# Performance work log

Hardware: AMD Instinct MI355X
Metric: run time of the kernel (lower is better)

Reference implementation:

```python
import jax, jax.numpy as jnp
import numpy as np

EPS = 1e-12


def _segment_softmax(logits, seg, n):
    # numerically stable softmax over edges grouped by destination node
    m = jax.ops.segment_max(logits, seg, num_segments=n)
    e = jnp.exp(logits - m[seg])
    s = jax.ops.segment_sum(e, seg, num_segments=n)
    return e / s[seg]


def _agnn(x, src, dst, beta, n):
    # cosine-similarity attention (PyG AGNNConv): alpha_ij = softmax_i(beta * <x_i/|x_i|, x_j/|x_j|>)
    norm = jnp.sqrt(jnp.sum(x * x, axis=-1, keepdims=True))
    xn = x / jnp.maximum(norm, EPS)
    logits = beta * jnp.sum(xn[dst] * xn[src], axis=-1)  # [E+N]
    alpha = _segment_softmax(logits, dst, n)
    return jax.ops.segment_sum(alpha[:, None] * x[src], dst, num_segments=n)


def setup_inputs() -> dict:
    key = jax.random.key(0)
    ks = jax.random.split(key, 6)
    N, E, F, H, C = 100000, 3200000, 512, 16, 7
    x = jax.random.normal(ks[0], (N, F), dtype=jnp.float32)
    edge_index = jax.random.randint(ks[1], (2, E), 0, N, dtype=jnp.int32)
    W1 = jax.random.normal(ks[2], (H, F), dtype=jnp.float32) * 0.05
    b1 = jnp.zeros((H,), jnp.float32)
    W2 = jax.random.normal(ks[3], (C, H), dtype=jnp.float32) * 0.2
    b2 = jnp.zeros((C,), jnp.float32)
    return {
        "x": x, "edge_index": edge_index,
        "W1": W1, "b1": b1,
        "beta2": jnp.ones((1,), jnp.float32),
        "beta3": jnp.ones((1,), jnp.float32),
        "beta4": jnp.ones((1,), jnp.float32),
        "W2": W2, "b2": b2,
    }


def reference(x, edge_index, W1, b1, beta2, beta3, beta4, W2, b2):
    N = x.shape[0]
    loop = jnp.arange(N, dtype=edge_index.dtype)
    src = jnp.concatenate([edge_index[0], loop])  # self-loops added by AGNNConv
    dst = jnp.concatenate([edge_index[1], loop])

    h = jax.nn.relu(x @ W1.T + b1)                 # lin1 on raw features (eval: dropout = id)
    h = _agnn(h, src, dst, jnp.float32(1.0), N)    # prop1: beta fixed at 1 (requires_grad=False)
    h = _agnn(h, src, dst, beta2[0], N)
    h = _agnn(h, src, dst, beta3[0], N)
    h = _agnn(h, src, dst, beta4[0], N)
    logits = h @ W2.T + b2
    return jax.nn.log_softmax(logits, axis=1)
```

## Files before the change

kernel.cpp:

```cpp
#include <hip/hip_runtime.h>
#include <hip/hip_fp16.h>
#include <math.h>

#define F 512
#define H 16
#define C 7
#define NB 512
#define BIN_CHUNK 4096
#define BIN_T 512

typedef _Float16 h2 __attribute__((ext_vector_type(2)));

__device__ __forceinline__ h2 as_h2(unsigned u) { return __builtin_bit_cast(h2, u); }
__device__ __forceinline__ unsigned as_u32(h2 v) { return __builtin_bit_cast(unsigned, v); }

__device__ __forceinline__ float dot2acc(h2 a, h2 b, float c) {
#if __has_builtin(__builtin_amdgcn_fdot2)
    return __builtin_amdgcn_fdot2(a, b, c, false);
#else
    return c + (float)a[0] * (float)b[0] + (float)a[1] * (float)b[1];
#endif
}

__global__ void zero_i32(int* p, int n) {
    int i = blockIdx.x * blockDim.x + threadIdx.x;
    if (i < n) p[i] = 0;
}

__global__ __launch_bounds__(BIN_T) void bin_edges(const int* __restrict__ ei, int E, int Etot,
                                                   int width, int cap, int* __restrict__ gcnt,
                                                   unsigned* __restrict__ binned) {
    __shared__ int cnt[NB];
    __shared__ int base[NB];
    int t = threadIdx.x;
    for (int i = t; i < NB; i += BIN_T) cnt[i] = 0;
    __syncthreads();
    long chunk0 = (long)blockIdx.x * BIN_CHUNK;
    for (int k = 0; k < BIN_CHUNK / BIN_T; ++k) {
        long e = chunk0 + k * BIN_T + t;
        if (e < Etot) {
            int dst = (e < E) ? ei[E + e] : (int)(e - E);
            atomicAdd(&cnt[dst / width], 1);
        }
    }
    __syncthreads();
    for (int i = t; i < NB; i += BIN_T) {
        int c = cnt[i];
        base[i] = c ? atomicAdd(&gcnt[i], c) : 0;
        cnt[i] = 0;
    }
    __syncthreads();
    for (int k = 0; k < BIN_CHUNK / BIN_T; ++k) {
        long e = chunk0 + k * BIN_T + t;
        if (e < Etot) {
            int src, dst;
            if (e < E) { src = ei[e]; dst = ei[E + e]; }
            else       { src = (int)(e - E); dst = src; }
            int b = dst / width;
            size_t pos = (size_t)b * cap + base[b] + atomicAdd(&cnt[b], 1);
            binned[pos] = (unsigned)src | ((unsigned)(dst - b * width) << 17);
        }
    }
}

__global__ void bucket_scan(const int* __restrict__ gcnt, int Etot,
                            int* __restrict__ bbase, int* __restrict__ rp, int N) {
    __shared__ int s[NB];
    int t = threadIdx.x;
    int own = gcnt[t];
    s[t] = own;
    __syncthreads();
    for (int d = 1; d < NB; d <<= 1) {
        int add = (t >= d) ? s[t - d] : 0;
        __syncthreads();
        s[t] += add;
        __syncthreads();
    }
    bbase[t] = s[t] - own;
    if (t == NB - 1) bbase[NB] = s[t];
    if (t == 0) rp[N] = Etot;
}

__global__ __launch_bounds__(256) void bucket_sort(const unsigned* __restrict__ binned,
                                                   const int* __restrict__ gcnt,
                                                   const int* __restrict__ bbase,
                                                   int width, int cap, int N,
                                                   int* __restrict__ rp, int* __restrict__ srcs) {
    __shared__ int cnt[256];
    __shared__ int cur[256];
    int b = blockIdx.x, t = threadIdx.x;
    int r0 = bbase[b];
    int ne = gcnt[b];
    const unsigned* bin = binned + (size_t)b * cap;
    int nodeBase = b * width;
    cnt[t] = 0;
    cur[t] = 0;
    __syncthreads();
    for (int e = t; e < ne; e += 256) {
        atomicAdd(&cnt[bin[e] >> 17], 1);
    }
    __syncthreads();
    int own = cnt[t];
    for (int d = 1; d < 256; d <<= 1) {
        int add = (t >= d) ? cnt[t - d] : 0;
        __syncthreads();
        cnt[t] += add;
        __syncthreads();
    }
    int excl = cnt[t] - own;
    int node = nodeBase + t;
    if (t < width && node < N) rp[node] = r0 + excl;
    __syncthreads();
    cnt[t] = excl;
    __syncthreads();
    for (int e = t; e < ne; e += 256) {
        unsigned p = bin[e];
        int dL = p >> 17;
        int pos = r0 + cnt[dL] + atomicAdd(&cur[dL], 1);
        srcs[pos] = (int)(p & 0x1FFFFu);
    }
}

__global__ __launch_bounds__(256) void lin1_relu(const float* __restrict__ x,
                                                 const float* __restrict__ W1,
                                                 const float* __restrict__ b1,
                                                 __half* __restrict__ hrow, int N) {
    __shared__ float4 w4[16 * 16 * 9];
    int t = threadIdx.x;
    for (int r = 0; r < 8; ++r) {
        int idx = r * 256 + t;
        int j = idx >> 7;
        int rem = idx & 127;
        int s = rem >> 3, m = rem & 7;
        w4[(j * 16 + s) * 9 + m] = ((const float4*)W1)[idx];
    }
    __syncthreads();

    int s = t & 15, g = t >> 4;
    int iA = blockIdx.x * 32 + g;
    int iB = iA + 16;
    int iAc = min(iA, N - 1), iBc = min(iB, N - 1);

    const float4* xA4 = (const float4*)(x + (size_t)iAc * F);
    const float4* xB4 = (const float4*)(x + (size_t)iBc * F);
    float4 xa[8], xb[8];
#pragma unroll
    for (int m = 0; m < 8; ++m) xa[m] = xA4[s * 8 + m];
#pragma unroll
    for (int m = 0; m < 8; ++m) xb[m] = xB4[s * 8 + m];

    float vA[16], vB[16];
#pragma unroll
    for (int j = 0; j < 16; ++j) { vA[j] = 0.f; vB[j] = 0.f; }
#pragma unroll
    for (int j = 0; j < 16; ++j) {
        const float4* wr = &w4[(j * 16 + s) * 9];
#pragma unroll
        for (int m = 0; m < 8; ++m) {
            float4 w = wr[m];
            vA[j] += w.x * xa[m].x + w.y * xa[m].y + w.z * xa[m].z + w.w * xa[m].w;
            vB[j] += w.x * xb[m].x + w.y * xb[m].y + w.z * xb[m].z + w.w * xb[m].w;
        }
    }

#pragma unroll
    for (int st = 0; st < 4; ++st) {
        int bit = (s >> st) & 1;
        int cntj = 16 >> (st + 1);
#pragma unroll
        for (int k = 0; k < 8; ++k) {
            if (k < cntj) {
                float keepA = bit ? vA[2 * k + 1] : vA[2 * k];
                float giveA = bit ? vA[2 * k] : vA[2 * k + 1];
                vA[k] = keepA + __shfl_xor(giveA, 1 << st);
                float keepB = bit ? vB[2 * k + 1] : vB[2 * k];
                float giveB = bit ? vB[2 * k] : vB[2 * k + 1];
                vB[k] = keepB + __shfl_xor(giveB, 1 << st);
            }
        }
    }

    float bs = b1[s];
    float oA = fmaxf(vA[0] + bs, 0.f);
    float oB = fmaxf(vB[0] + bs, 0.f);

    float sqA = oA * oA, sqB = oB * oB;
    sqA += __shfl_xor(sqA, 1); sqA += __shfl_xor(sqA, 2);
    sqA += __shfl_xor(sqA, 4); sqA += __shfl_xor(sqA, 8);
    sqB += __shfl_xor(sqB, 1); sqB += __shfl_xor(sqB, 2);
    sqB += __shfl_xor(sqB, 4); sqB += __shfl_xor(sqB, 8);
    float rnA = 1.0f / fmaxf(sqrtf(sqA), 1e-12f);
    float rnB = 1.0f / fmaxf(sqrtf(sqB), 1e-12f);

    if (iA < N) {
        hrow[(size_t)iA * 32 + s] = __float2half(oA * rnA);
        hrow[(size_t)iA * 32 + 16 + s] = __float2half(oA);
    }
    if (iB < N) {
        hrow[(size_t)iB * 32 + s] = __float2half(oB * rnB);
        hrow[(size_t)iB * 32 + 16 + s] = __float2half(oB);
    }
}

__global__ __launch_bounds__(256) void agnn_step(const uint4* __restrict__ hrow,
                                                 const int* __restrict__ rp,
                                                 const int* __restrict__ srcs,
                                                 const float* __restrict__ bp,
                                                 uint4* __restrict__ hrow_out, int N) {
    int t = threadIdx.x;
    int sub = t & 3, g = t >> 2;
    int i = blockIdx.x * 64 + g;
    if (i >= N) return;

    const float L2E = 1.4426950408889634f;
    float beta = bp ? bp[0] : 1.0f;
    float aL = beta * L2E;
    float mm = fabsf(beta) * L2E;

    uint4 hA = hrow[(size_t)i * 4 + 0];
    uint4 hB = hrow[(size_t)i * 4 + 1];
    h2 hi[8];
    hi[0] = as_h2(hA.x); hi[1] = as_h2(hA.y); hi[2] = as_h2(hA.z); hi[3] = as_h2(hA.w);
    hi[4] = as_h2(hB.x); hi[5] = as_h2(hB.y); hi[6] = as_h2(hB.z); hi[7] = as_h2(hB.w);

    int e0 = rp[i];
    int deg = rp[i + 1] - e0;
    int dm1 = deg - 1;
    int U = (deg + 3) >> 2;

    int sbuf[4];
    uint4 rbuf[4][4];
#pragma unroll
    for (int u = 0; u < 4; ++u) {
        int s = srcs[e0 + min(sub + 4 * u, dm1)];
        const uint4* r = hrow + (size_t)s * 4;
        rbuf[u][0] = r[0]; rbuf[u][1] = r[1]; rbuf[u][2] = r[2]; rbuf[u][3] = r[3];
        sbuf[u] = srcs[e0 + min(sub + 4 * (u + 4), dm1)];
    }

    float denom = 0.f;
    float acc[16];
#pragma unroll
    for (int j = 0; j < 16; ++j) acc[j] = 0.f;

    for (int mb = 0; mb < U; mb += 4) {
#pragma unroll
        for (int u = 0; u < 4; ++u) {
            int m = mb + u;
            int k = sub + 4 * m;
            uint4 a = rbuf[u][0], b = rbuf[u][1], c = rbuf[u][2], d = rbuf[u][3];
            int snext = sbuf[u];
            sbuf[u] = srcs[e0 + min(sub + 4 * (m + 8), dm1)];
            const uint4* r = hrow + (size_t)snext * 4;
            rbuf[u][0] = r[0]; rbuf[u][1] = r[1]; rbuf[u][2] = r[2]; rbuf[u][3] = r[3];

            float dot = 0.f;
            dot = dot2acc(hi[0], as_h2(a.x), dot);
            dot = dot2acc(hi[1], as_h2(a.y), dot);
            dot = dot2acc(hi[2], as_h2(a.z), dot);
            dot = dot2acc(hi[3], as_h2(a.w), dot);
            dot = dot2acc(hi[4], as_h2(b.x), dot);
            dot = dot2acc(hi[5], as_h2(b.y), dot);
            dot = dot2acc(hi[6], as_h2(b.z), dot);
            dot = dot2acc(hi[7], as_h2(b.w), dot);

            float w = exp2f(fmaf(aL, dot, -mm));
            w = (k < deg) ? w : 0.f;
            denom += w;

            h2 c0 = as_h2(c.x), c1 = as_h2(c.y), c2 = as_h2(c.z), c3 = as_h2(c.w);
            h2 d0 = as_h2(d.x), d1 = as_h2(d.y), d2 = as_h2(d.z), d3 = as_h2(d.w);
            acc[0]  = fmaf(w, (float)c0[0], acc[0]);
            acc[1]  = fmaf(w, (float)c0[1], acc[1]);
            acc[2]  = fmaf(w, (float)c1[0], acc[2]);
            acc[3]  = fmaf(w, (float)c1[1], acc[3]);
            acc[4]  = fmaf(w, (float)c2[0], acc[4]);
            acc[5]  = fmaf(w, (float)c2[1], acc[5]);
            acc[6]  = fmaf(w, (float)c3[0], acc[6]);
            acc[7]  = fmaf(w, (float)c3[1], acc[7]);
            acc[8]  = fmaf(w, (float)d0[0], acc[8]);
            acc[9]  = fmaf(w, (float)d0[1], acc[9]);
            acc[10] = fmaf(w, (float)d1[0], acc[10]);
            acc[11] = fmaf(w, (float)d1[1], acc[11]);
            acc[12] = fmaf(w, (float)d2[0], acc[12]);
            acc[13] = fmaf(w, (float)d2[1], acc[13]);
            acc[14] = fmaf(w, (float)d3[0], acc[14]);
            acc[15] = fmaf(w, (float)d3[1], acc[15]);
        }
    }

    denom += __shfl_xor(denom, 1);
    denom += __shfl_xor(denom, 2);
#pragma unroll
    for (int j = 0; j < 16; ++j) {
        acc[j] += __shfl_xor(acc[j], 1);
        acc[j] += __shfl_xor(acc[j], 2);
    }

    float rd = 1.0f / denom;
    float o[16];
    float sq = 0.f;
#pragma unroll
    for (int j = 0; j < 16; ++j) {
        o[j] = acc[j] * rd;
        sq = fmaf(o[j], o[j], sq);
    }
    float rno = 1.0f / fmaxf(sqrtf(sq), 1e-12f);

    float scale = (sub < 2) ? rno : 1.0f;
    int half = (sub & 1) * 8;
    uint4 wq;
    {
        h2 t0, t1;
        t0[0] = (_Float16)(o[half + 0] * scale); t0[1] = (_Float16)(o[half + 1] * scale);
        t1[0] = (_Float16)(o[half + 2] * scale); t1[1] = (_Float16)(o[half + 3] * scale);
        wq.x = as_u32(t0); wq.y = as_u32(t1);
        t0[0] = (_Float16)(o[half + 4] * scale); t0[1] = (_Float16)(o[half + 5] * scale);
        t1[0] = (_Float16)(o[half + 6] * scale); t1[1] = (_Float16)(o[half + 7] * scale);
        wq.z = as_u32(t0); wq.w = as_u32(t1);
    }
    hrow_out[(size_t)i * 4 + sub] = wq;
}

__global__ __launch_bounds__(256) void head_kernel(const uint4* __restrict__ hrow,
                                                   const float* __restrict__ W2,
                                                   const float* __restrict__ b2,
                                                   float* __restrict__ out, int N) {
    __shared__ float w2[C * H];
    __shared__ float bb[C];
    int t = threadIdx.x;
    if (t < C * H) w2[t] = W2[t];
    if (t < C) bb[t] = b2[t];
    __syncthreads();
    int i = blockIdx.x * blockDim.x + t;
    if (i >= N) return;
    uint4 cA = hrow[(size_t)i * 4 + 2];
    uint4 cB = hrow[(size_t)i * 4 + 3];
    float hv[H];
    {
        h2 v;
        v = as_h2(cA.x); hv[0] = (float)v[0];  hv[1] = (float)v[1];
        v = as_h2(cA.y); hv[2] = (float)v[0];  hv[3] = (float)v[1];
        v = as_h2(cA.z); hv[4] = (float)v[0];  hv[5] = (float)v[1];
        v = as_h2(cA.w); hv[6] = (float)v[0];  hv[7] = (float)v[1];
        v = as_h2(cB.x); hv[8] = (float)v[0];  hv[9] = (float)v[1];
        v = as_h2(cB.y); hv[10] = (float)v[0]; hv[11] = (float)v[1];
        v = as_h2(cB.z); hv[12] = (float)v[0]; hv[13] = (float)v[1];
        v = as_h2(cB.w); hv[14] = (float)v[0]; hv[15] = (float)v[1];
    }
    float lg[C];
    float m = -1e30f;
#pragma unroll
    for (int c = 0; c < C; ++c) {
        float s = bb[c];
#pragma unroll
        for (int k = 0; k < H; ++k) s += hv[k] * w2[c * H + k];
        lg[c] = s;
        m = fmaxf(m, s);
    }
    float sum = 0.f;
#pragma unroll
    for (int c = 0; c < C; ++c) sum += expf(lg[c] - m);
    float lse = m + logf(sum);
    float* op = out + (size_t)i * C;
#pragma unroll
    for (int c = 0; c < C; ++c) op[c] = lg[c] - lse;
}

extern "C" void kernel_launch(void* const* d_in, const int* in_sizes, int n_in,
                              void* d_out, int out_size, void* d_ws, size_t ws_size,
                              hipStream_t stream) {
    const float* x     = (const float*)d_in[0];
    const int*   ei    = (const int*)d_in[1];
    const float* W1    = (const float*)d_in[2];
    const float* b1    = (const float*)d_in[3];
    const float* beta2 = (const float*)d_in[4];
    const float* beta3 = (const float*)d_in[5];
    const float* beta4 = (const float*)d_in[6];
    const float* W2    = (const float*)d_in[7];
    const float* b2    = (const float*)d_in[8];
    float* out = (float*)d_out;

    int N = in_sizes[0] / F;
    int E = in_sizes[1] / 2;
    int Etot = E + N;
    int width = (N + NB - 1) / NB;
    int cap = (Etot / NB) * 5 / 4;

    char* p = (char*)d_ws;
    uint4* hr_a = (uint4*)p; p += (size_t)N * 64;
    uint4* hr_b = (uint4*)p; p += (size_t)N * 64;
    int* rp     = (int*)p;   p += (size_t)(N + 1) * 4;
    int* srcs   = (int*)p;   p += (size_t)Etot * 4;
    int* gcnt   = (int*)p;   p += (size_t)NB * 4;
    int* bbase  = (int*)p;   p += (size_t)(NB + 1) * 4;
    p = (char*)(((size_t)p + 255) & ~(size_t)255);
    unsigned* binned = (unsigned*)p; p += (size_t)NB * cap * 4;

    zero_i32<<<(NB + 255) / 256, 256, 0, stream>>>(gcnt, NB);
    bin_edges<<<(Etot + BIN_CHUNK - 1) / BIN_CHUNK, BIN_T, 0, stream>>>(ei, E, Etot, width, cap, gcnt, binned);
    bucket_scan<<<1, NB, 0, stream>>>(gcnt, Etot, bbase, rp, N);
    bucket_sort<<<NB, 256, 0, stream>>>(binned, gcnt, bbase, width, cap, N, rp, srcs);

    lin1_relu<<<(N + 31) / 32, 256, 0, stream>>>(x, W1, b1, (__half*)hr_a, N);

    int gs = (N + 63) / 64;
    agnn_step<<<gs, 256, 0, stream>>>(hr_a, rp, srcs, nullptr, hr_b, N);
    agnn_step<<<gs, 256, 0, stream>>>(hr_b, rp, srcs, beta2, hr_a, N);
    agnn_step<<<gs, 256, 0, stream>>>(hr_a, rp, srcs, beta3, hr_b, N);
    agnn_step<<<gs, 256, 0, stream>>>(hr_b, rp, srcs, beta4, hr_a, N);

    head_kernel<<<(N + 255) / 256, 256, 0, stream>>>(hr_a, W2, b2, out, N);
}
```

Measured before the change: 590.8 us.

## Split each neighbor row across four lanes in AGNN step instead of per-edge lanes

Changes agnn_step so the four lanes of a node cooperatively load one 64-byte neighbor row (one uint4 each), with the source index broadcast by shuffle. The normalized-half dot product is split across lanes 0/1 and combined by shuffles, and each lane accumulates 8 output features instead of 16. The cross-lane reduction at the end is dropped. This aims to get coalesced row loads and lower register pressure, at the cost of many more shuffles per edge and a two-stage prefetch instead of the deeper four-row lookahead.

```diff
diff --git a/kernel.cpp b/kernel.cpp
--- a/kernel.cpp
+++ b/kernel.cpp
@@ -211,6 +211,7 @@
     int sub = t & 3, g = t >> 2;
     int i = blockIdx.x * 64 + g;
     if (i >= N) return;
+    int base = (t & 63) & ~3;
 
     const float L2E = 1.4426950408889634f;
     float beta = bp ? bp[0] : 1.0f;
@@ -223,100 +224,96 @@
     hi[0] = as_h2(hA.x); hi[1] = as_h2(hA.y); hi[2] = as_h2(hA.z); hi[3] = as_h2(hA.w);
     hi[4] = as_h2(hB.x); hi[5] = as_h2(hB.y); hi[6] = as_h2(hB.z); hi[7] = as_h2(hB.w);
 
+    h2 hiq[4];
+    bool odd = (sub & 1);
+#pragma unroll
+    for (int q = 0; q < 4; ++q) hiq[q] = odd ? hi[4 + q] : hi[q];
+
     int e0 = rp[i];
     int deg = rp[i + 1] - e0;
     int dm1 = deg - 1;
     int U = (deg + 3) >> 2;
 
-    int sbuf[4];
-    uint4 rbuf[4][4];
-#pragma unroll
-    for (int u = 0; u < 4; ++u) {
-        int s = srcs[e0 + min(sub + 4 * u, dm1)];
-        const uint4* r = hrow + (size_t)s * 4;
-        rbuf[u][0] = r[0]; rbuf[u][1] = r[1]; rbuf[u][2] = r[2]; rbuf[u][3] = r[3];
-        sbuf[u] = srcs[e0 + min(sub + 4 * (u + 4), dm1)];
+    int sv_cur = srcs[e0 + min(sub, dm1)];
+    int sv_nxt = srcs[e0 + min(4 + sub, dm1)];
+    uint4 rcur[4];
+#pragma unroll
+    for (int j = 0; j < 4; ++j) {
+        int sj = __shfl(sv_cur, base + j, 64);
+        rcur[j] = hrow[(size_t)sj * 4 + sub];
     }
 
     float denom = 0.f;
-    float acc[16];
-#pragma unroll
-    for (int j = 0; j < 16; ++j) acc[j] = 0.f;
-
-    for (int mb = 0; mb < U; mb += 4) {
-#pragma unroll
-        for (int u = 0; u < 4; ++u) {
-            int m = mb + u;
-            int k = sub + 4 * m;
-            uint4 a = rbuf[u][0], b = rbuf[u][1], c = rbuf[u][2], d = rbuf[u][3];
-            int snext = sbuf[u];
-            sbuf[u] = srcs[e0 + min(sub + 4 * (m + 8), dm1)];
-            const uint4* r = hrow + (size_t)snext * 4;
-            rbuf[u][0] = r[0]; rbuf[u][1] = r[1]; rbuf[u][2] = r[2]; rbuf[u][3] = r[3];
-
-            float dot = 0.f;
-            dot = dot2acc(hi[0], as_h2(a.x), dot);
-            dot = dot2acc(hi[1], as_h2(a.y), dot);
-            dot = dot2acc(hi[2], as_h2(a.z), dot);
-            dot = dot2acc(hi[3], as_h2(a.w), dot);
-            dot = dot2acc(hi[4], as_h2(b.x), dot);
-            dot = dot2acc(hi[5], as_h2(b.y), dot);
-            dot = dot2acc(hi[6], as_h2(b.z), dot);
-            dot = dot2acc(hi[7], as_h2(b.w), dot);
+    float acc[8];
+#pragma unroll
+    for (int j = 0; j < 8; ++j) acc[j] = 0.f;
+
+    for (int step = 0; step < U; ++step) {
+        uint4 rnxt[4];
+#pragma unroll
+        for (int j = 0; j < 4; ++j) {
+            int sj = __shfl(sv_nxt, base + j, 64);
+            rnxt[j] = hrow[(size_t)sj * 4 + sub];
+        }
+        int sv_n2 = srcs[e0 + min((step + 2) * 4 + sub, dm1)];
+
+#pragma unroll
+        for (int j = 0; j < 4; ++j) {
+            int k = 4 * step + j;
+            uint4 r = rcur[j];
+            h2 r0 = as_h2(r.x), r1 = as_h2(r.y), r2 = as_h2(r.z), r3 = as_h2(r.w);
+
+            float part = 0.f;
+            part = dot2acc(hiq[0], r0, part);
+            part = dot2acc(hiq[1], r1, part);
+            part = dot2acc(hiq[2], r2, part);
+            part = dot2acc(hiq[3], r3, part);
+            float dot = __shfl(part, base + 0, 64) + __shfl(part, base + 1, 64);
 
             float w = exp2f(fmaf(aL, dot, -mm));
             w = (k < deg) ? w : 0.f;
             denom += w;
 
-            h2 c0 = as_h2(c.x), c1 = as_h2(c.y), c2 = as_h2(c.z), c3 = as_h2(c.w);
-            h2 d0 = as_h2(d.x), d1 = as_h2(d.y), d2 = as_h2(d.z), d3 = as_h2(d.w);
-            acc[0]  = fmaf(w, (float)c0[0], acc[0]);
-            acc[1]  = fmaf(w, (float)c0[1], acc[1]);
-            acc[2]  = fmaf(w, (float)c1[0], acc[2]);
-            acc[3]  = fmaf(w, (float)c1[1], acc[3]);
-            acc[4]  = fmaf(w, (float)c2[0], acc[4]);
-            acc[5]  = fmaf(w, (float)c2[1], acc[5]);
-            acc[6]  = fmaf(w, (float)c3[0], acc[6]);
-            acc[7]  = fmaf(w, (float)c3[1], acc[7]);
-            acc[8]  = fmaf(w, (float)d0[0], acc[8]);
-            acc[9]  = fmaf(w, (float)d0[1], acc[9]);
-            acc[10] = fmaf(w, (float)d1[0], acc[10]);
-            acc[11] = fmaf(w, (float)d1[1], acc[11]);
-            acc[12] = fmaf(w, (float)d2[0], acc[12]);
-            acc[13] = fmaf(w, (float)d2[1], acc[13]);
-            acc[14] = fmaf(w, (float)d3[0], acc[14]);
-            acc[15] = fmaf(w, (float)d3[1], acc[15]);
-        }
-    }
-
-    denom += __shfl_xor(denom, 1);
-    denom += __shfl_xor(denom, 2);
-#pragma unroll
-    for (int j = 0; j < 16; ++j) {
-        acc[j] += __shfl_xor(acc[j], 1);
-        acc[j] += __shfl_xor(acc[j], 2);
+            acc[0] = fmaf(w, (float)r0[0], acc[0]);
+            acc[1] = fmaf(w, (float)r0[1], acc[1]);
+            acc[2] = fmaf(w, (float)r1[0], acc[2]);
+            acc[3] = fmaf(w, (float)r1[1], acc[3]);
+            acc[4] = fmaf(w, (float)r2[0], acc[4]);
+            acc[5] = fmaf(w, (float)r2[1], acc[5]);
+            acc[6] = fmaf(w, (float)r3[0], acc[6]);
+            acc[7] = fmaf(w, (float)r3[1], acc[7]);
+        }
+
+#pragma unroll
+        for (int j = 0; j < 4; ++j) rcur[j] = rnxt[j];
+        sv_nxt = sv_n2;
     }
 
     float rd = 1.0f / denom;
-    float o[16];
-    float sq = 0.f;
-#pragma unroll
-    for (int j = 0; j < 16; ++j) {
+    float o[8];
+    float sq8 = 0.f;
+#pragma unroll
+    for (int j = 0; j < 8; ++j) {
         o[j] = acc[j] * rd;
-        sq = fmaf(o[j], o[j], sq);
-    }
+        sq8 = fmaf(o[j], o[j], sq8);
+    }
+    float sq = __shfl(sq8, base + 2, 64) + __shfl(sq8, base + 3, 64);
     float rno = 1.0f / fmaxf(sqrtf(sq), 1e-12f);
 
+    int srcl = base + 2 + (sub & 1);
     float scale = (sub < 2) ? rno : 1.0f;
-    int half = (sub & 1) * 8;
     uint4 wq;
     {
         h2 t0, t1;
-        t0[0] = (_Float16)(o[half + 0] * scale); t0[1] = (_Float16)(o[half + 1] * scale);
-        t1[0] = (_Float16)(o[half + 2] * scale); t1[1] = (_Float16)(o[half + 3] * scale);
+        float v0 = __shfl(o[0], srcl, 64), v1 = __shfl(o[1], srcl, 64);
+        float v2 = __shfl(o[2], srcl, 64), v3 = __shfl(o[3], srcl, 64);
+        t0[0] = (_Float16)(v0 * scale); t0[1] = (_Float16)(v1 * scale);
+        t1[0] = (_Float16)(v2 * scale); t1[1] = (_Float16)(v3 * scale);
         wq.x = as_u32(t0); wq.y = as_u32(t1);
-        t0[0] = (_Float16)(o[half + 4] * scale); t0[1] = (_Float16)(o[half + 5] * scale);
-        t1[0] = (_Float16)(o[half + 6] * scale); t1[1] = (_Float16)(o[half + 7] * scale);
+        float v4 = __shfl(o[4], srcl, 64), v5 = __shfl(o[5], srcl, 64);
+        float v6 = __shfl(o[6], srcl, 64), v7 = __shfl(o[7], srcl, 64);
+        t0[0] = (_Float16)(v4 * scale); t0[1] = (_Float16)(v5 * scale);
+        t1[0] = (_Float16)(v6 * scale); t1[1] = (_Float16)(v7 * scale);
         wq.z = as_u32(t0); wq.w = as_u32(t1);
     }
     hrow_out[(size_t)i * 4 + sub] = wq;
```

Result: slower. 653.1 us (+10.6%).

## Sort nodes by degree to balance per-wave work in AGNN steps

Applied to the files above, without the earlier changes.

Adds a degree histogram, a scan and a placement pass that build a permutation of nodes ordered by in-degree. Each agnn_step then processes nodes in that order, so the 16 nodes sharing a wave have similar edge counts and lanes idle less. The cost is three extra small kernels and an extra indirection, which leaves per-node row reads and writes non-sequential.

```diff
diff --git a/kernel.cpp b/kernel.cpp
--- a/kernel.cpp
+++ b/kernel.cpp
@@ -6,6 +6,7 @@
 #define H 16
 #define C 7
 #define NB 512
+#define DB 256
 #define BIN_CHUNK 4096
 #define BIN_T 512
 
@@ -121,6 +122,54 @@
     }
 }
 
+__global__ __launch_bounds__(256) void deg_hist(const int* __restrict__ rp, int N,
+                                                int* __restrict__ dcnt) {
+    __shared__ int c[DB];
+    int t = threadIdx.x;
+    c[t] = 0;
+    __syncthreads();
+    for (int i = blockIdx.x * 256 + t; i < N; i += gridDim.x * 256) {
+        int d = min(rp[i + 1] - rp[i], DB - 1);
+        atomicAdd(&c[d], 1);
+    }
+    __syncthreads();
+    if (c[t]) atomicAdd(&dcnt[t], c[t]);
+}
+
+__global__ void deg_scan(const int* __restrict__ dcnt, int* __restrict__ dpos) {
+    __shared__ int s[DB];
+    int t = threadIdx.x;
+    int own = dcnt[t];
+    s[t] = own;
+    __syncthreads();
+    for (int d = 1; d < DB; d <<= 1) {
+        int add = (t >= d) ? s[t - d] : 0;
+        __syncthreads();
+        s[t] += add;
+        __syncthreads();
+    }
+    dpos[t] = s[t] - own;
+}
+
+__global__ __launch_bounds__(256) void deg_place(const int* __restrict__ rp, int N,
+                                                 int* __restrict__ dpos, int* __restrict__ perm) {
+    __shared__ int c[DB];
+    __shared__ int b[DB];
+    int t = threadIdx.x;
+    c[t] = 0;
+    __syncthreads();
+    int i = blockIdx.x * 256 + t;
+    int d = 0, loff = 0;
+    if (i < N) {
+        d = min(rp[i + 1] - rp[i], DB - 1);
+        loff = atomicAdd(&c[d], 1);
+    }
+    __syncthreads();
+    if (c[t]) b[t] = atomicAdd(&dpos[t], c[t]);
+    __syncthreads();
+    if (i < N) perm[b[d] + loff] = i;
+}
+
 __global__ __launch_bounds__(256) void lin1_relu(const float* __restrict__ x,
                                                  const float* __restrict__ W1,
                                                  const float* __restrict__ b1,
@@ -205,12 +254,14 @@
 __global__ __launch_bounds__(256) void agnn_step(const uint4* __restrict__ hrow,
                                                  const int* __restrict__ rp,
                                                  const int* __restrict__ srcs,
+                                                 const int* __restrict__ perm,
                                                  const float* __restrict__ bp,
                                                  uint4* __restrict__ hrow_out, int N) {
     int t = threadIdx.x;
     int sub = t & 3, g = t >> 2;
-    int i = blockIdx.x * 64 + g;
-    if (i >= N) return;
+    int ii = blockIdx.x * 64 + g;
+    if (ii >= N) return;
+    int i = perm[ii];
 
     const float L2E = 1.4426950408889634f;
     float beta = bp ? bp[0] : 1.0f;
@@ -392,23 +443,30 @@
     uint4* hr_b = (uint4*)p; p += (size_t)N * 64;
     int* rp     = (int*)p;   p += (size_t)(N + 1) * 4;
     int* srcs   = (int*)p;   p += (size_t)Etot * 4;
+    int* perm   = (int*)p;   p += (size_t)N * 4;
     int* gcnt   = (int*)p;   p += (size_t)NB * 4;
+    int* dcnt   = (int*)p;   p += (size_t)DB * 4;
+    int* dpos   = (int*)p;   p += (size_t)DB * 4;
     int* bbase  = (int*)p;   p += (size_t)(NB + 1) * 4;
     p = (char*)(((size_t)p + 255) & ~(size_t)255);
     unsigned* binned = (unsigned*)p; p += (size_t)NB * cap * 4;
 
-    zero_i32<<<(NB + 255) / 256, 256, 0, stream>>>(gcnt, NB);
+    zero_i32<<<(NB + DB + 255) / 256, 256, 0, stream>>>(gcnt, NB + DB);
     bin_edges<<<(Etot + BIN_CHUNK - 1) / BIN_CHUNK, BIN_T, 0, stream>>>(ei, E, Etot, width, cap, gcnt, binned);
     bucket_scan<<<1, NB, 0, stream>>>(gcnt, Etot, bbase, rp, N);
     bucket_sort<<<NB, 256, 0, stream>>>(binned, gcnt, bbase, width, cap, N, rp, srcs);
 
+    deg_hist<<<128, 256, 0, stream>>>(rp, N, dcnt);
+    deg_scan<<<1, DB, 0, stream>>>(dcnt, dpos);
+    deg_place<<<(N + 255) / 256, 256, 0, stream>>>(rp, N, dpos, perm);
+
     lin1_relu<<<(N + 31) / 32, 256, 0, stream>>>(x, W1, b1, (__half*)hr_a, N);
 
     int gs = (N + 63) / 64;
-    agnn_step<<<gs, 256, 0, stream>>>(hr_a, rp, srcs, nullptr, hr_b, N);
-    agnn_step<<<gs, 256, 0, stream>>>(hr_b, rp, srcs, beta2, hr_a, N);
-    agnn_step<<<gs, 256, 0, stream>>>(hr_a, rp, srcs, beta3, hr_b, N);
-    agnn_step<<<gs, 256, 0, stream>>>(hr_b, rp, srcs, beta4, hr_a, N);
+    agnn_step<<<gs, 256, 0, stream>>>(hr_a, rp, srcs, perm, nullptr, hr_b, N);
+    agnn_step<<<gs, 256, 0, stream>>>(hr_b, rp, srcs, perm, beta2, hr_a, N);
+    agnn_step<<<gs, 256, 0, stream>>>(hr_a, rp, srcs, perm, beta3, hr_b, N);
+    agnn_step<<<gs, 256, 0, stream>>>(hr_b, rp, srcs, perm, beta4, hr_a, N);
 
     head_kernel<<<(N + 255) / 256, 256, 0, stream>>>(hr_a, W2, b2, out, N);
 }
```

After: 618.5 us. 4.7% more time.
